# Performance work log

Hardware: AMD Instinct MI355X
Metric: run time of the kernel (lower is better)

## Reference

```python
import jax, jax.numpy as jnp
import numpy as np

B, S, E = 2048, 23, 768
RED, H, NUM_LABELS = 256, 8, 25
DH = RED // H
DELTA = 0.1
EPS_LN = 1e-5


def setup_inputs() -> dict:
    key = jax.random.key(0)
    ks = jax.random.split(key, 20)
    g = lambda k, shape, fan: jax.random.normal(k, shape, dtype=jnp.float32) * (1.0 / np.sqrt(fan))
    inp = {
        'cls_embeddings': jax.random.normal(ks[0], (B, S, E), dtype=jnp.float32),
        'existing_mask': jax.random.randint(ks[1], (B, S), 0, 2, dtype=jnp.int32),
        'missing_emb': g(ks[2], (S, E), E),
        'W1': g(ks[3], (E // 2, E), E), 'b1': jnp.zeros((E // 2,), jnp.float32),
        'W2': g(ks[4], (RED, E // 2), E // 2), 'b2': jnp.zeros((RED,), jnp.float32),
        'ln_g': jnp.ones((RED,), jnp.float32), 'ln_b': jnp.zeros((RED,), jnp.float32),
        'Wq': g(ks[5], (RED, RED), RED), 'bq': jnp.zeros((RED,), jnp.float32),
        'Wk': g(ks[6], (RED, RED), RED), 'bk': jnp.zeros((RED,), jnp.float32),
        'Wv': g(ks[7], (RED, RED), RED), 'bv': jnp.zeros((RED,), jnp.float32),
        'Wo': g(ks[8], (RED, RED), RED), 'bo': jnp.zeros((RED,), jnp.float32),
        'Wp': g(ks[9], (NUM_LABELS, RED), RED), 'bp': jnp.zeros((NUM_LABELS,), jnp.float32),
    }
    return inp


def _layer_norm(x, g, b):
    mu = jnp.mean(x, axis=-1, keepdims=True)
    var = jnp.mean(jnp.square(x - mu), axis=-1, keepdims=True)
    return (x - mu) * jax.lax.rsqrt(var + EPS_LN) * g + b


def _forward(cls_embeddings, existing_mask, missing_emb, W1, b1, W2, b2, ln_g, ln_b,
             Wq, bq, Wk, bk, Wv, bv, Wo, bo, Wp, bp):
    exist = existing_mask > 0                              # [B,S] bool
    # Gather: existing sections use BERT CLS, missing slots use learned embeddings
    sec = jnp.where(exist[..., None], cls_embeddings, missing_emb[None])  # [B,S,E]
    # SectionDimReducer (exact-erf GELU as in nn.GELU default)
    h = jax.nn.gelu(sec @ W1.T + b1, approximate=False)
    h = jax.nn.gelu(h @ W2.T + b2, approximate=False)
    red = _layer_norm(h, ln_g, ln_b)                       # [B,S,RED]
    # Tiny MHA: every slot queries the existing sections of its own EHR
    q = (red @ Wq.T + bq).reshape(B, S, H, DH)
    k = (red @ Wk.T + bk).reshape(B, S, H, DH)
    v = (red @ Wv.T + bv).reshape(B, S, H, DH)
    scores = jnp.einsum('bqhd,bkhd->bhqk', q, k) / np.sqrt(DH)
    scores = jnp.where(exist[:, None, None, :], scores, -1e9)
    attn = jax.nn.softmax(scores, axis=-1)                 # [B,H,S,S]
    ctx = jnp.einsum('bhqk,bkhd->bqhd', attn, v).reshape(B, S, RED)
    mha_out = ctx @ Wo.T + bo                              # [B,S,RED]
    # Scatter: only missing slots (of EHRs with >=1 existing section) are replaced
    any_exist = jnp.any(exist, axis=1)                     # [B]
    use_attn = (~exist) & any_exist[:, None]               # [B,S]
    updated = jnp.where(use_attn[..., None], mha_out, red)
    # margin-based orthogonality loss on section embeddings
    norm = updated / jnp.maximum(jnp.linalg.norm(updated, axis=-1, keepdims=True), 1e-8)
    gram = jnp.einsum('bid,bjd->bij', norm, norm)          # [B,S,S]
    off = 1.0 - jnp.eye(S, dtype=updated.dtype)
    loss_orth = jnp.sum(jax.nn.relu(jnp.abs(gram) - DELTA) * off) / (B * S * (S - 1))
    logits = updated.mean(axis=1) @ Wp.T + bp              # [B,NUM_LABELS]
    return loss_orth, logits


def reference(cls_embeddings, existing_mask, missing_emb, W1, b1, W2, b2, ln_g, ln_b,
              Wq, bq, Wk, bk, Wv, bv, Wo, bo, Wp, bp):
    return _forward(cls_embeddings, existing_mask, missing_emb, W1, b1, W2, b2, ln_g, ln_b,
                    Wq, bq, Wk, bk, Wv, bv, Wo, bo, Wp, bp)
```

## Files before the change

### kernel.cpp

```cpp
#include <hip/hip_runtime.h>

typedef unsigned short u16;
typedef unsigned int u32;
typedef __attribute__((ext_vector_type(8))) short short8;
typedef __attribute__((ext_vector_type(4))) float f32x4;

struct __align__(8) us4 { u16 x, y, z, w; };

__device__ __forceinline__ float bf1(u16 v){ return __uint_as_float(((u32)v) << 16); }
__device__ __forceinline__ float bflo(u32 u){ return __uint_as_float(u << 16); }
__device__ __forceinline__ float bfhi(u32 u){ return __uint_as_float(u & 0xFFFF0000u); }
__device__ __forceinline__ u16 fbf(float f){
    u32 u = __float_as_uint(f);
    return (u16)((u + 0x7FFFu + ((u >> 16) & 1u)) >> 16);
}
__device__ __forceinline__ float gelu_exact(float x){
    return 0.5f * x * (1.0f + erff(x * 0.70710678118654752f));
}
__device__ __forceinline__ void unp8(uint4 u, float* f){
    f[0]=bflo(u.x); f[1]=bfhi(u.x); f[2]=bflo(u.y); f[3]=bfhi(u.y);
    f[4]=bflo(u.z); f[5]=bfhi(u.z); f[6]=bflo(u.w); f[7]=bfhi(u.w);
}
__device__ __forceinline__ uint4 pack8(float4 a, float4 b){
    uint4 u;
    u.x = (u32)fbf(a.x) | ((u32)fbf(a.y) << 16);
    u.y = (u32)fbf(a.z) | ((u32)fbf(a.w) << 16);
    u.z = (u32)fbf(b.x) | ((u32)fbf(b.y) << 16);
    u.w = (u32)fbf(b.z) | ((u32)fbf(b.w) << 16);
    return u;
}


__global__ __launch_bounds__(256) void wconv(
    const float* __restrict__ W1, const float* __restrict__ W2,
    const float* __restrict__ Wq, const float* __restrict__ Wk,
    const float* __restrict__ Wv, const float* __restrict__ Wo,
    const float* __restrict__ Wp, u16* __restrict__ dst)
{
    const int i = blockIdx.x * 256 + threadIdx.x;
    const float* s; int o;
    if      (i < 294912) { s = W1; o = i; }
    else if (i < 393216) { s = W2; o = i - 294912; }
    else if (i < 458752) { s = Wq; o = i - 393216; }
    else if (i < 524288) { s = Wk; o = i - 458752; }
    else if (i < 589824) { s = Wv; o = i - 524288; }
    else if (i < 655360) { s = Wo; o = i - 589824; }
    else                 { s = Wp; o = i - 655360; }
    dst[i] = fbf(s[o]);
}

__global__ __launch_bounds__(256) void gemm1_kernel(
    const float* __restrict__ cls, const int* __restrict__ mask,
    const float* __restrict__ missing, const u16* __restrict__ W,
    const float* __restrict__ bias, u16* __restrict__ C)
{
    const int K = 768, M = 384;
    __shared__ u16 As[128 * 40];
    __shared__ u16 Bs[128 * 40];
    const int tid = threadIdx.x;
    const int w = tid >> 6, lane = tid & 63;
    const int nBase = blockIdx.y * 128, mBase = blockIdx.x * 128;
    const int wr = w >> 1, wc = w & 1;
    const int r0 = tid >> 2;
    const int co = (tid & 3) * 8;
    const int frow = lane & 15, quad = lane >> 4;

    const int rowA0 = nBase + r0, rowA1 = nBase + r0 + 64;
    const float* ap0 = (mask[rowA0] > 0) ? cls + (size_t)rowA0 * 768
                                         : missing + (size_t)(rowA0 % 23) * 768;
    const float* ap1 = (mask[rowA1] > 0) ? cls + (size_t)rowA1 * 768
                                         : missing + (size_t)(rowA1 % 23) * 768;
    const u16* bp0 = W + (size_t)(mBase + r0) * K;
    const u16* bp1 = W + (size_t)(mBase + r0 + 64) * K;

    f32x4 acc[4][4];
#pragma unroll
    for (int mt = 0; mt < 4; ++mt)
#pragma unroll
        for (int nt = 0; nt < 4; ++nt) acc[mt][nt] = f32x4{0.f, 0.f, 0.f, 0.f};

    float4 a0a = *(const float4*)(ap0 + co), a0b = *(const float4*)(ap0 + co + 4);
    float4 a1a = *(const float4*)(ap1 + co), a1b = *(const float4*)(ap1 + co + 4);
    uint4 pb0 = *(const uint4*)(bp0 + co), pb1 = *(const uint4*)(bp1 + co);

    for (int k0 = 0; k0 < K; k0 += 32) {
        __syncthreads();
        *(uint4*)(As + r0 * 40 + co) = pack8(a0a, a0b);
        *(uint4*)(As + (r0 + 64) * 40 + co) = pack8(a1a, a1b);
        *(uint4*)(Bs + r0 * 40 + co) = pb0;
        *(uint4*)(Bs + (r0 + 64) * 40 + co) = pb1;
        __syncthreads();
        if (k0 + 32 < K) {
            const int kn = k0 + 32 + co;
            a0a = *(const float4*)(ap0 + kn); a0b = *(const float4*)(ap0 + kn + 4);
            a1a = *(const float4*)(ap1 + kn); a1b = *(const float4*)(ap1 + kn + 4);
            pb0 = *(const uint4*)(bp0 + kn);  pb1 = *(const uint4*)(bp1 + kn);
        }
        short8 af[4], bfv[4];
#pragma unroll
        for (int mt = 0; mt < 4; ++mt)
            af[mt] = *(const short8*)(As + (wr * 64 + mt * 16 + frow) * 40 + quad * 8);
#pragma unroll
        for (int nt = 0; nt < 4; ++nt)
            bfv[nt] = *(const short8*)(Bs + (wc * 64 + nt * 16 + frow) * 40 + quad * 8);
#pragma unroll
        for (int mt = 0; mt < 4; ++mt)
#pragma unroll
            for (int nt = 0; nt < 4; ++nt)
                acc[mt][nt] = __builtin_amdgcn_mfma_f32_16x16x32_bf16(
                    af[mt], bfv[nt], acc[mt][nt], 0, 0, 0);
    }

#pragma unroll
    for (int nt = 0; nt < 4; ++nt) {
        const int col = mBase + wc * 64 + nt * 16 + frow;
        const float bv = bias[col];
#pragma unroll
        for (int mt = 0; mt < 4; ++mt)
#pragma unroll
            for (int reg = 0; reg < 4; ++reg) {
                const int row = nBase + wr * 64 + mt * 16 + quad * 4 + reg;
                C[(size_t)row * M + col] = fbf(gelu_exact(acc[mt][nt][reg] + bv));
            }
    }
}

__global__ __launch_bounds__(256) void gemm_bt(
    const u16* __restrict__ A, const u16* __restrict__ W,
    const float* __restrict__ bias, u16* __restrict__ C, int K, int M)
{
    __shared__ u16 As[128 * 40];
    __shared__ u16 Bs[128 * 40];
    const int tid = threadIdx.x;
    const int w = tid >> 6, lane = tid & 63;
    const int nBase = blockIdx.y * 128, mBase = blockIdx.x * 128;
    const int wr = w >> 1, wc = w & 1;
    const int r0 = tid >> 2;
    const int co = (tid & 3) * 8;
    const int frow = lane & 15, quad = lane >> 4;

    f32x4 acc[4][4];
#pragma unroll
    for (int mt = 0; mt < 4; ++mt)
#pragma unroll
        for (int nt = 0; nt < 4; ++nt) acc[mt][nt] = f32x4{0.f, 0.f, 0.f, 0.f};

    uint4 pa0 = *(const uint4*)(A + (size_t)(nBase + r0) * K + co);
    uint4 pa1 = *(const uint4*)(A + (size_t)(nBase + r0 + 64) * K + co);
    uint4 pb0 = *(const uint4*)(W + (size_t)(mBase + r0) * K + co);
    uint4 pb1 = *(const uint4*)(W + (size_t)(mBase + r0 + 64) * K + co);

    for (int k0 = 0; k0 < K; k0 += 32) {
        __syncthreads();
        *(uint4*)(As + r0 * 40 + co) = pa0;
        *(uint4*)(As + (r0 + 64) * 40 + co) = pa1;
        *(uint4*)(Bs + r0 * 40 + co) = pb0;
        *(uint4*)(Bs + (r0 + 64) * 40 + co) = pb1;
        __syncthreads();
        if (k0 + 32 < K) {
            const int kn = k0 + 32 + co;
            pa0 = *(const uint4*)(A + (size_t)(nBase + r0) * K + kn);
            pa1 = *(const uint4*)(A + (size_t)(nBase + r0 + 64) * K + kn);
            pb0 = *(const uint4*)(W + (size_t)(mBase + r0) * K + kn);
            pb1 = *(const uint4*)(W + (size_t)(mBase + r0 + 64) * K + kn);
        }
        short8 af[4], bfv[4];
#pragma unroll
        for (int mt = 0; mt < 4; ++mt)
            af[mt] = *(const short8*)(As + (wr * 64 + mt * 16 + frow) * 40 + quad * 8);
#pragma unroll
        for (int nt = 0; nt < 4; ++nt)
            bfv[nt] = *(const short8*)(Bs + (wc * 64 + nt * 16 + frow) * 40 + quad * 8);
#pragma unroll
        for (int mt = 0; mt < 4; ++mt)
#pragma unroll
            for (int nt = 0; nt < 4; ++nt)
                acc[mt][nt] = __builtin_amdgcn_mfma_f32_16x16x32_bf16(
                    af[mt], bfv[nt], acc[mt][nt], 0, 0, 0);
    }

#pragma unroll
    for (int nt = 0; nt < 4; ++nt) {
        const int col = mBase + wc * 64 + nt * 16 + frow;
        const float bv = bias[col];
#pragma unroll
        for (int mt = 0; mt < 4; ++mt)
#pragma unroll
            for (int reg = 0; reg < 4; ++reg) {
                const int row = nBase + wr * 64 + mt * 16 + quad * 4 + reg;
                C[(size_t)row * M + col] = fbf(gelu_exact(acc[mt][nt][reg] + bv));
            }
    }
}

__global__ __launch_bounds__(256) void ln_kernel(
    u16* __restrict__ X, const float* __restrict__ g, const float* __restrict__ b)
{
    const int w = threadIdx.x >> 6, lane = threadIdx.x & 63;
    const size_t row = (size_t)blockIdx.x * 4 + w;
    u16* xp = X + row * 256 + lane * 4;
    us4 uv = *(const us4*)xp;
    float x0 = bf1(uv.x), x1 = bf1(uv.y), x2 = bf1(uv.z), x3 = bf1(uv.w);
    float s = x0 + x1 + x2 + x3;
#pragma unroll
    for (int m = 32; m; m >>= 1) s += __shfl_xor(s, m);
    const float mu = s * (1.f / 256.f);
    const float d0 = x0 - mu, d1 = x1 - mu, d2 = x2 - mu, d3 = x3 - mu;
    float vs = d0 * d0 + d1 * d1 + d2 * d2 + d3 * d3;
#pragma unroll
    for (int m = 32; m; m >>= 1) vs += __shfl_xor(vs, m);
    const float rs = rsqrtf(vs * (1.f / 256.f) + 1e-5f);
    const float4 gv = *(const float4*)(g + lane * 4);
    const float4 bv = *(const float4*)(b + lane * 4);
    us4 o;
    o.x = fbf(d0 * rs * gv.x + bv.x);
    o.y = fbf(d1 * rs * gv.y + bv.y);
    o.z = fbf(d2 * rs * gv.z + bv.z);
    o.w = fbf(d3 * rs * gv.w + bv.w);
    *(us4*)xp = o;
}

#define QSTR 264
__global__ __launch_bounds__(256) void attn1_kernel(
    u16* __restrict__ redb, const int* __restrict__ mask,
    const u16* __restrict__ Wqkvb,
    const float* __restrict__ bq, const float* __restrict__ bk,
    const float* __restrict__ bv, const u16* __restrict__ Wob,
    const float* __restrict__ bo)
{
    __shared__ __align__(16) unsigned char SM[44896];
    u16* s_rq = (u16*)SM;
    u16* s_k  = (u16*)(SM + 12144);
    u16* s_v  = (u16*)(SM + 24288);
    u16* s_p  = (u16*)(SM + 36064);
    __shared__ int sEx[23];
    __shared__ int sMiss[23];

    const int b = blockIdx.x, t = threadIdx.x;
    const int w = t >> 6, lane = t & 63;
    const int frow = lane & 15, quad = lane >> 4;
    const int r0c = frow;
    const int r1c = (16 + frow > 22) ? 22 : 16 + frow;

    if (t < 23) sEx[t] = mask[b * 23 + t];
    __syncthreads();
    if (t == 0) {
        int any = 0;
        for (int s = 0; s < 23; ++s) any |= (sEx[s] > 0) ? 1 : 0;
        for (int s = 0; s < 23; ++s) sMiss[s] = (any && sEx[s] <= 0) ? 1 : 0;
    }
    for (int i = t; i < 736; i += 256) {
        const int s = i >> 5, c8 = (i & 31) * 8;
        *(uint4*)(s_rq + s * QSTR + c8) =
            *(const uint4*)(redb + ((size_t)(b * 23 + s)) * 256 + c8);
    }
    __syncthreads();

    {
        f32x4 qacc[2][12];
#pragma unroll
        for (int mt = 0; mt < 2; ++mt)
#pragma unroll
            for (int nt = 0; nt < 12; ++nt) qacc[mt][nt] = f32x4{0.f, 0.f, 0.f, 0.f};
        for (int k0 = 0; k0 < 256; k0 += 32) {
            short8 a0 = *(const short8*)(s_rq + r0c * QSTR + k0 + quad * 8);
            short8 a1 = *(const short8*)(s_rq + r1c * QSTR + k0 + quad * 8);
#pragma unroll
            for (int nt = 0; nt < 12; ++nt) {
                const int n = w * 192 + nt * 16 + frow;
                short8 bfr = *(const short8*)(Wqkvb + (size_t)n * 256 + k0 + quad * 8);
                qacc[0][nt] = __builtin_amdgcn_mfma_f32_16x16x32_bf16(a0, bfr, qacc[0][nt], 0, 0, 0);
                qacc[1][nt] = __builtin_amdgcn_mfma_f32_16x16x32_bf16(a1, bfr, qacc[1][nt], 0, 0, 0);
            }
        }
        __syncthreads();
#pragma unroll
        for (int mt = 0; mt < 2; ++mt)
#pragma unroll
            for (int nt = 0; nt < 12; ++nt) {
                const int col = w * 192 + nt * 16 + frow;
                const int seg = col >> 8, cm = col & 255;
                const float bb = (seg == 0) ? bq[cm] : (seg == 1) ? bk[cm] : bv[cm];
#pragma unroll
                for (int reg = 0; reg < 4; ++reg) {
                    const int s = mt * 16 + quad * 4 + reg;
                    if (s < 23) {
                        const u16 hv = fbf(qacc[mt][nt][reg] + bb);
                        if (seg == 0)      s_rq[s * QSTR + cm] = hv;
                        else if (seg == 1) s_k[s * QSTR + cm] = hv;
                        else               s_v[s * 256 + cm] = hv;
                    }
                }
            }
    }
    __syncthreads();

    if (t < 184) {
        const int hh = t / 23, qi = t - hh * 23;
        const u16* qrow = s_rq + qi * QSTR + hh * 32;
        float qf[32];
#pragma unroll
        for (int c8 = 0; c8 < 4; ++c8) unp8(*(const uint4*)(qrow + c8 * 8), qf + c8 * 8);
        float p[23];
        float mx = -1e30f;
#pragma unroll
        for (int j = 0; j < 23; ++j) {
            const u16* krow = s_k + j * QSTR + hh * 32;
            float sc = 0.f;
#pragma unroll
            for (int c8 = 0; c8 < 4; ++c8) {
                float kf[8]; unp8(*(const uint4*)(krow + c8 * 8), kf);
#pragma unroll
                for (int e = 0; e < 8; ++e) sc += qf[c8 * 8 + e] * kf[e];
            }
            sc *= 0.17677669529663687f;
            if (sEx[j] <= 0) sc = -1e9f;
            p[j] = sc; mx = fmaxf(mx, sc);
        }
        float sum = 0.f;
#pragma unroll
        for (int j = 0; j < 23; ++j) { p[j] = expf(p[j] - mx); sum += p[j]; }
        const float inv = 1.f / sum;
#pragma unroll
        for (int j = 0; j < 23; ++j) s_p[(hh * 23 + qi) * 24 + j] = fbf(p[j] * inv);
    }
    __syncthreads();

    {
        const int d = t, h = t >> 5;
        float vreg[23];
#pragma unroll
        for (int j = 0; j < 23; ++j) vreg[j] = bf1(s_v[j * 256 + d]);
#pragma unroll
        for (int s = 0; s < 23; ++s) {
            float a = 0.f;
            const u16* pr = s_p + (h * 23 + s) * 24;
#pragma unroll
            for (int j = 0; j < 23; ++j) a += bf1(pr[j]) * vreg[j];
            s_k[s * QSTR + d] = fbf(a);
        }
    }
    __syncthreads();

    {
        f32x4 wacc[2][4];
#pragma unroll
        for (int mt = 0; mt < 2; ++mt)
#pragma unroll
            for (int nt = 0; nt < 4; ++nt) wacc[mt][nt] = f32x4{0.f, 0.f, 0.f, 0.f};
        for (int k0 = 0; k0 < 256; k0 += 32) {
            short8 a0 = *(const short8*)(s_k + r0c * QSTR + k0 + quad * 8);
            short8 a1 = *(const short8*)(s_k + r1c * QSTR + k0 + quad * 8);
#pragma unroll
            for (int nt = 0; nt < 4; ++nt) {
                const int n = w * 64 + nt * 16 + frow;
                short8 bfr = *(const short8*)(Wob + (size_t)n * 256 + k0 + quad * 8);
                wacc[0][nt] = __builtin_amdgcn_mfma_f32_16x16x32_bf16(a0, bfr, wacc[0][nt], 0, 0, 0);
                wacc[1][nt] = __builtin_amdgcn_mfma_f32_16x16x32_bf16(a1, bfr, wacc[1][nt], 0, 0, 0);
            }
        }
#pragma unroll
        for (int mt = 0; mt < 2; ++mt)
#pragma unroll
            for (int nt = 0; nt < 4; ++nt) {
                const int col = w * 64 + nt * 16 + frow;
                const float bvv = bo[col];
#pragma unroll
                for (int reg = 0; reg < 4; ++reg) {
                    const int s = mt * 16 + quad * 4 + reg;
                    if (s < 23 && sMiss[s])
                        redb[((size_t)(b * 23 + s)) * 256 + col] =
                            fbf(wacc[mt][nt][reg] + bvv);
                }
            }
    }
}

__global__ __launch_bounds__(256) void tail_kernel(
    const u16* __restrict__ redb, const u16* __restrict__ Wpb,
    const float* __restrict__ bp, float* __restrict__ out,
    float* __restrict__ lossAcc)
{
    __shared__ __align__(16) u16 s_u[23 * QSTR];
    __shared__ float sInv[23];
    __shared__ float sPool[256];
    __shared__ float sRsc[4];

    const int b = blockIdx.x, t = threadIdx.x;
    const int w = t >> 6, lane = t & 63;

    for (int i = t; i < 736; i += 256) {
        const int s = i >> 5, c8 = (i & 31) * 8;
        *(uint4*)(s_u + s * QSTR + c8) =
            *(const uint4*)(redb + ((size_t)(b * 23 + s)) * 256 + c8);
    }
    __syncthreads();

    if (t < 23) {
        float ss = 0.f;
        for (int c8 = 0; c8 < 32; ++c8) {
            float rf[8]; unp8(*(const uint4*)(s_u + t * QSTR + c8 * 8), rf);
#pragma unroll
            for (int e = 0; e < 8; ++e) ss += rf[e] * rf[e];
        }
        sInv[t] = 1.f / fmaxf(sqrtf(ss), 1e-8f);
    }
    __syncthreads();

    {
        float contrib = 0.f;
        if (t < 253) {
            int i = 0, rem = t, cnt = 22;
            while (rem >= cnt) { rem -= cnt; --cnt; ++i; }
            const int j = i + 1 + rem;
            float dp = 0.f;
            for (int c8 = 0; c8 < 32; ++c8) {
                float fa[8], fb[8];
                unp8(*(const uint4*)(s_u + i * QSTR + c8 * 8), fa);
                unp8(*(const uint4*)(s_u + j * QSTR + c8 * 8), fb);
#pragma unroll
                for (int e = 0; e < 8; ++e) dp += fa[e] * fb[e];
            }
            const float g = dp * sInv[i] * sInv[j];
            const float c = fabsf(g) - 0.1f;
            contrib = (c > 0.f) ? 2.f * c : 0.f;
        }
#pragma unroll
        for (int m = 32; m; m >>= 1) contrib += __shfl_xor(contrib, m);
        if (lane == 0) sRsc[w] = contrib;
        __syncthreads();
        if (t == 0) atomicAdd(lossAcc, sRsc[0] + sRsc[1] + sRsc[2] + sRsc[3]);
    }

    {
        float pv = 0.f;
#pragma unroll
        for (int s = 0; s < 23; ++s) pv += bf1(s_u[s * QSTR + t]);
        sPool[t] = pv * (1.f / 23.f);
    }
    __syncthreads();
    if (t < 25) {
        float a = bp[t];
        for (int c8 = 0; c8 < 32; ++c8) {
            float wf[8]; unp8(*(const uint4*)(Wpb + (size_t)t * 256 + c8 * 8), wf);
            const float4 p0 = *(const float4*)(sPool + c8 * 8);
            const float4 p1 = *(const float4*)(sPool + c8 * 8 + 4);
            a += wf[0] * p0.x + wf[1] * p0.y + wf[2] * p0.z + wf[3] * p0.w
               + wf[4] * p1.x + wf[5] * p1.y + wf[6] * p1.z + wf[7] * p1.w;
        }
        out[1 + b * 25 + t] = a;
    }
}

__global__ void loss_finalize(const float* __restrict__ lossAcc, float* __restrict__ out)
{
    out[0] = lossAcc[0] * (1.f / 1036288.f);
}

extern "C" void kernel_launch(void* const* d_in, const int* in_sizes, int n_in,
                              void* d_out, int out_size, void* d_ws, size_t ws_size,
                              hipStream_t stream)
{
    const float* cls     = (const float*)d_in[0];
    const int*   mask    = (const int*)d_in[1];
    const float* missing = (const float*)d_in[2];
    const float* W1 = (const float*)d_in[3];  const float* b1 = (const float*)d_in[4];
    const float* W2 = (const float*)d_in[5];  const float* b2 = (const float*)d_in[6];
    const float* lng = (const float*)d_in[7]; const float* lnb = (const float*)d_in[8];
    const float* Wq = (const float*)d_in[9];  const float* bq = (const float*)d_in[10];
    const float* Wk = (const float*)d_in[11]; const float* bk = (const float*)d_in[12];
    const float* Wv = (const float*)d_in[13]; const float* bv = (const float*)d_in[14];
    const float* Wo = (const float*)d_in[15]; const float* bo = (const float*)d_in[16];
    const float* Wp = (const float*)d_in[17]; const float* bp = (const float*)d_in[18];
    float* out = (float*)d_out;

    char* ws = (char*)d_ws;
    u16* h1b  = (u16*)ws;
    u16* redb = (u16*)(ws + 36175872);
    u16* Wb   = (u16*)(ws + 60293120);
    u16* W1b   = Wb;
    u16* W2b   = Wb + 294912;
    u16* Wqkvb = Wb + 393216;
    u16* Wob   = Wb + 589824;
    u16* Wpb   = Wb + 655360;
    float* lossAcc = (float*)(ws + 61616640);

    hipMemsetAsync(lossAcc, 0, sizeof(float), stream);

    wconv<<<2585, 256, 0, stream>>>(W1, W2, Wq, Wk, Wv, Wo, Wp, Wb);
    gemm1_kernel<<<dim3(3, 368), 256, 0, stream>>>(cls, mask, missing, W1b, b1, h1b);
    gemm_bt<<<dim3(2, 368), 256, 0, stream>>>(h1b, W2b, b2, redb, 384, 256);
    ln_kernel<<<11776, 256, 0, stream>>>(redb, lng, lnb);
    attn1_kernel<<<2048, 256, 0, stream>>>(redb, mask, Wqkvb, bq, bk, bv, Wob, bo);
    tail_kernel<<<2048, 256, 0, stream>>>(redb, Wpb, bp, out, lossAcc);
    loss_finalize<<<1, 1, 0, stream>>>(lossAcc, out);
}
```

Measured before the change: 608.0 us.

## Compute attention scores and PV with MFMA and in-register shuffle softmax

Replaces the scalar per-thread QK^T dot products, softmax and PV accumulation in the attention kernel with bf16 MFMA tiles per head. Each wave handles two heads, does the row softmax with cross-lane shuffles, and stores V transposed and zero-padded in shared memory so it can feed MFMA directly. This removes a barrier and the separate probability buffer, and uses all threads rather than 184 for the score stage. In exchange it adds a fast exp, bf16 rounding of probabilities inside the MFMA path, and in-place reuse of the K and Q buffers.

Measured after the change: 593.9 us. 1.02x faster.

```diff
diff --git a/kernel.cpp b/kernel.cpp
--- a/kernel.cpp
+++ b/kernel.cpp
@@ -228,13 +228,13 @@
     const float* __restrict__ bv, const u16* __restrict__ Wob,
     const float* __restrict__ bo)
 {
-    __shared__ __align__(16) unsigned char SM[44896];
+    __shared__ __align__(16) unsigned char SM[44768];
     u16* s_rq = (u16*)SM;
     u16* s_k  = (u16*)(SM + 12144);
-    u16* s_v  = (u16*)(SM + 24288);
-    u16* s_p  = (u16*)(SM + 36064);
+    u16* s_vT = (u16*)(SM + 24288);
     __shared__ int sEx[23];
     __shared__ int sMiss[23];
+    __shared__ float sMaskF[32];
 
     const int b = blockIdx.x, t = threadIdx.x;
     const int w = t >> 6, lane = t & 63;
@@ -249,6 +249,8 @@
         for (int s = 0; s < 23; ++s) any |= (sEx[s] > 0) ? 1 : 0;
         for (int s = 0; s < 23; ++s) sMiss[s] = (any && sEx[s] <= 0) ? 1 : 0;
     }
+    if (t < 32) sMaskF[t] = (t < 23 && sEx[t] > 0) ? 0.f : -1e9f;
+    for (int i = t; i < 1280; i += 256) ((uint4*)s_vT)[i] = make_uint4(0u, 0u, 0u, 0u);
     for (int i = t; i < 736; i += 256) {
         const int s = i >> 5, c8 = (i & 31) * 8;
         *(uint4*)(s_rq + s * QSTR + c8) =
@@ -288,56 +290,79 @@
                         const u16 hv = fbf(qacc[mt][nt][reg] + bb);
                         if (seg == 0)      s_rq[s * QSTR + cm] = hv;
                         else if (seg == 1) s_k[s * QSTR + cm] = hv;
-                        else               s_v[s * 256 + cm] = hv;
+                        else               s_vT[cm * 40 + s] = hv;
                     }
                 }
             }
     }
     __syncthreads();
 
-    if (t < 184) {
-        const int hh = t / 23, qi = t - hh * 23;
-        const u16* qrow = s_rq + qi * QSTR + hh * 32;
-        float qf[32];
-#pragma unroll
-        for (int c8 = 0; c8 < 4; ++c8) unp8(*(const uint4*)(qrow + c8 * 8), qf + c8 * 8);
-        float p[23];
-        float mx = -1e30f;
-#pragma unroll
-        for (int j = 0; j < 23; ++j) {
-            const u16* krow = s_k + j * QSTR + hh * 32;
-            float sc = 0.f;
-#pragma unroll
-            for (int c8 = 0; c8 < 4; ++c8) {
-                float kf[8]; unp8(*(const uint4*)(krow + c8 * 8), kf);
-#pragma unroll
-                for (int e = 0; e < 8; ++e) sc += qf[c8 * 8 + e] * kf[e];
-            }
-            sc *= 0.17677669529663687f;
-            if (sEx[j] <= 0) sc = -1e9f;
-            p[j] = sc; mx = fmaxf(mx, sc);
-        }
-        float sum = 0.f;
-#pragma unroll
-        for (int j = 0; j < 23; ++j) { p[j] = expf(p[j] - mx); sum += p[j]; }
-        const float inv = 1.f / sum;
-#pragma unroll
-        for (int j = 0; j < 23; ++j) s_p[(hh * 23 + qi) * 24 + j] = fbf(p[j] * inv);
-    }
-    __syncthreads();
-
     {
-        const int d = t, h = t >> 5;
-        float vreg[23];
-#pragma unroll
-        for (int j = 0; j < 23; ++j) vreg[j] = bf1(s_v[j * 256 + d]);
-#pragma unroll
-        for (int s = 0; s < 23; ++s) {
-            float a = 0.f;
-            const u16* pr = s_p + (h * 23 + s) * 24;
-#pragma unroll
-            for (int j = 0; j < 23; ++j) a += bf1(pr[j]) * vreg[j];
-            s_k[s * QSTR + d] = fbf(a);
+        const float scl = 0.17677669529663687f;
+        const float m0 = sMaskF[frow];
+        const float m1 = sMaskF[16 + frow];
+        const f32x4 z4 = f32x4{0.f, 0.f, 0.f, 0.f};
+#pragma unroll
+        for (int hh2 = 0; hh2 < 2; ++hh2) {
+            const int hb = (w * 2 + hh2) * 32;
+            short8 aq0 = *(const short8*)(s_rq + r0c * QSTR + hb + quad * 8);
+            short8 aq1 = *(const short8*)(s_rq + r1c * QSTR + hb + quad * 8);
+            short8 bk0 = *(const short8*)(s_k + r0c * QSTR + hb + quad * 8);
+            short8 bk1 = *(const short8*)(s_k + r1c * QSTR + hb + quad * 8);
+            f32x4 s00 = __builtin_amdgcn_mfma_f32_16x16x32_bf16(aq0, bk0, z4, 0, 0, 0);
+            f32x4 s01 = __builtin_amdgcn_mfma_f32_16x16x32_bf16(aq0, bk1, z4, 0, 0, 0);
+            f32x4 s10 = __builtin_amdgcn_mfma_f32_16x16x32_bf16(aq1, bk0, z4, 0, 0, 0);
+            f32x4 s11 = __builtin_amdgcn_mfma_f32_16x16x32_bf16(aq1, bk1, z4, 0, 0, 0);
+#pragma unroll
+            for (int mt = 0; mt < 2; ++mt) {
+                f32x4& c0 = mt ? s10 : s00;
+                f32x4& c1 = mt ? s11 : s01;
+#pragma unroll
+                for (int reg = 0; reg < 4; ++reg) {
+                    float v0 = c0[reg] * scl + m0;
+                    float v1 = c1[reg] * scl + m1;
+                    float mx = fmaxf(v0, v1);
+#pragma unroll
+                    for (int m = 8; m; m >>= 1) mx = fmaxf(mx, __shfl_xor(mx, m));
+                    float p0 = __expf(v0 - mx), p1 = __expf(v1 - mx);
+                    float sm = p0 + p1;
+#pragma unroll
+                    for (int m = 8; m; m >>= 1) sm += __shfl_xor(sm, m);
+                    const float inv = 1.f / sm;
+                    c0[reg] = p0 * inv;
+                    c1[reg] = p1 * inv;
+                }
+            }
+#pragma unroll
+            for (int reg = 0; reg < 4; ++reg) {
+                const int q0r = quad * 4 + reg;
+                s_k[q0r * QSTR + hb + frow]      = fbf(s00[reg]);
+                s_k[q0r * QSTR + hb + 16 + frow] = fbf(s01[reg]);
+                const int q1r = 16 + quad * 4 + reg;
+                if (q1r < 23) {
+                    s_k[q1r * QSTR + hb + frow]      = fbf(s10[reg]);
+                    s_k[q1r * QSTR + hb + 16 + frow] = fbf(s11[reg]);
+                }
+            }
+            short8 pa0 = *(const short8*)(s_k + r0c * QSTR + hb + quad * 8);
+            short8 pa1 = *(const short8*)(s_k + r1c * QSTR + hb + quad * 8);
+            short8 bv0 = *(const short8*)(s_vT + (hb + frow) * 40 + quad * 8);
+            short8 bv1 = *(const short8*)(s_vT + (hb + 16 + frow) * 40 + quad * 8);
+            f32x4 c00 = __builtin_amdgcn_mfma_f32_16x16x32_bf16(pa0, bv0, z4, 0, 0, 0);
+            f32x4 c01 = __builtin_amdgcn_mfma_f32_16x16x32_bf16(pa0, bv1, z4, 0, 0, 0);
+            f32x4 c10 = __builtin_amdgcn_mfma_f32_16x16x32_bf16(pa1, bv0, z4, 0, 0, 0);
+            f32x4 c11 = __builtin_amdgcn_mfma_f32_16x16x32_bf16(pa1, bv1, z4, 0, 0, 0);
+#pragma unroll
+            for (int reg = 0; reg < 4; ++reg) {
+                const int q0r = quad * 4 + reg;
+                s_rq[q0r * QSTR + hb + frow]      = fbf(c00[reg]);
+                s_rq[q0r * QSTR + hb + 16 + frow] = fbf(c01[reg]);
+                const int q1r = 16 + quad * 4 + reg;
+                if (q1r < 23) {
+                    s_rq[q1r * QSTR + hb + frow]      = fbf(c10[reg]);
+                    s_rq[q1r * QSTR + hb + 16 + frow] = fbf(c11[reg]);
+                }
+            }
         }
     }
     __syncthreads();
@@ -349,8 +374,8 @@
 #pragma unroll
             for (int nt = 0; nt < 4; ++nt) wacc[mt][nt] = f32x4{0.f, 0.f, 0.f, 0.f};
         for (int k0 = 0; k0 < 256; k0 += 32) {
-            short8 a0 = *(const short8*)(s_k + r0c * QSTR + k0 + quad * 8);
-            short8 a1 = *(const short8*)(s_k + r1c * QSTR + k0 + quad * 8);
+            short8 a0 = *(const short8*)(s_rq + r0c * QSTR + k0 + quad * 8);
+            short8 a1 = *(const short8*)(s_rq + r1c * QSTR + k0 + quad * 8);
 #pragma unroll
             for (int nt = 0; nt < 4; ++nt) {
                 const int n = w * 64 + nt * 16 + frow;
```
